# Optimization experiments

Measured on AMD Instinct MI355X. Metric: run time of the kernel, lower is better.

The kernel has to match this reference:

```python
import jax, jax.numpy as jnp
import numpy as np

B, IN, H, L = 128, 256, 1024, 256
nA, nB = H // 2, (H - 1) // 2        # pairs per A-layer / B-layer
LB = L // 2
LA = L - LB                           # A layers come first when L is odd
PI = float(np.pi)


def setup_inputs() -> dict:
    key = jax.random.key(0)
    ks = jax.random.split(key, 14)
    u = lambda k, shp: jax.random.uniform(k, shp, minval=-PI, maxval=PI)
    return {
        "inputsR": jax.random.normal(ks[0], (B, IN), dtype=jnp.float32),
        "inputsI": jax.random.normal(ks[1], (B, IN), dtype=jnp.float32),
        "stateR": jax.random.normal(ks[2], (B, H), dtype=jnp.float32),
        "stateI": jax.random.normal(ks[3], (B, H), dtype=jnp.float32),
        # CLinear params (init_scale=0.01 inside RNNCellCmplx)
        "weightR": 0.01 * jax.random.normal(ks[4], (H, IN), dtype=jnp.float32),
        "weightI": 0.01 * jax.random.normal(ks[5], (H, IN), dtype=jnp.float32),
        "biasR": 0.01 * jax.random.normal(ks[6], (H,), dtype=jnp.float32),
        "biasI": 0.01 * jax.random.normal(ks[7], (H,), dtype=jnp.float32),
        # Clements mesh angles, uniform(-pi, pi)
        "angleA0": u(ks[8], (LA, nA)),
        "angleA1": u(ks[9], (LA, nA)),
        "angleB0": u(ks[10], (LB, nB)),
        "angleB1": u(ks[11], (LB, nB)),
        # diagonal phase + modReLU bias (both init to zero)
        "omega": jnp.zeros((H,), dtype=jnp.float32),
        "mod_bias": jnp.zeros((H,), dtype=jnp.float32),
    }


def _mzi(ar, ai, br, bi, th0, th1):
    """PSDC MZI on channel pairs: phase shifter e^{i*th0} on arm a, then a
    directional coupler with coupling angle th1 (unitary 2x2)."""
    c0, s0 = jnp.cos(th0), jnp.sin(th0)
    pr = c0 * ar - s0 * ai          # p = e^{i th0} * a
    pi_ = s0 * ar + c0 * ai
    c, s = jnp.cos(th1), jnp.sin(th1)
    oar = c * pr - s * bi           # a' = cos*p + i sin*b
    oai = c * pi_ + s * br
    obr = c * br - s * pi_          # b' = i sin*p + cos*b
    obi = c * bi + s * pr
    return oar, oai, obr, obi


def _layerA(xr, xi, t0, t1):
    Bs, N = xr.shape
    oar, oai, obr, obi = _mzi(xr[:, 0::2], xi[:, 0::2], xr[:, 1::2], xi[:, 1::2], t0, t1)
    xr = jnp.stack([oar, obr], axis=-1).reshape(Bs, N)
    xi = jnp.stack([oai, obi], axis=-1).reshape(Bs, N)
    return xr, xi


def _layerB(xr, xi, t0, t1):
    Bs, N = xr.shape  # pairs (1,2),(3,4),... ; channels 0 and N-1 pass through
    oar, oai, obr, obi = _mzi(xr[:, 1:-1:2], xi[:, 1:-1:2], xr[:, 2::2], xi[:, 2::2], t0, t1)
    midr = jnp.stack([oar, obr], axis=-1).reshape(Bs, N - 2)
    midi = jnp.stack([oai, obi], axis=-1).reshape(Bs, N - 2)
    xr = jnp.concatenate([xr[:, :1], midr, xr[:, -1:]], axis=1)
    xi = jnp.concatenate([xi[:, :1], midi, xi[:, -1:]], axis=1)
    return xr, xi


def _clements(xr, xi, A0, A1, B0, B1):
    def step(carry, ang):
        cr, ci = carry
        a0, a1, b0, b1 = ang
        cr, ci = _layerA(cr, ci, a0, a1)
        cr, ci = _layerB(cr, ci, b0, b1)
        return (cr, ci), None
    (xr, xi), _ = jax.lax.scan(step, (xr, xi), (A0[:LB], A1[:LB], B0, B1))
    for k in range(LB, LA):  # trailing A layer when num_layers is odd (static)
        xr, xi = _layerA(xr, xi, A0[k], A1[k])
    return xr, xi


def _forward(inputsR, inputsI, stateR, stateI, weightR, weightI, biasR, biasI,
             angleA0, angleA1, angleB0, angleB1, omega, mod_bias):
    # CLinear: complex y = W x + b
    ihR = inputsR @ weightR.T - inputsI @ weightI.T + biasR
    ihI = inputsR @ weightI.T + inputsI @ weightR.T + biasI
    # Clements unitary mesh on hidden state
    hr, hi = _clements(stateR, stateI, angleA0, angleA1, angleB0, angleB1)
    # diagonal phase e^{i omega}
    co, so = jnp.cos(omega), jnp.sin(omega)
    hhR = co * hr - so * hi
    hhI = so * hr + co * hi
    # complex add
    zr = ihR + hhR
    zi = ihI + hhI
    # modReLU: relu(|z| + b) * z / |z|
    mag = jnp.sqrt(zr * zr + zi * zi)
    scale = jax.nn.relu(mag + mod_bias) / jnp.maximum(mag, 1e-8)
    return jnp.stack([scale * zr, scale * zi])  # (2, B, H)


def reference(inputsR, inputsI, stateR, stateI, weightR, weightI, biasR, biasI,
              angleA0, angleA1, angleB0, angleB1, omega, mod_bias):
    return _forward(inputsR, inputsI, stateR, stateI, weightR, weightI, biasR, biasI,
                    angleA0, angleA1, angleB0, angleB1, omega, mod_bias)
```

## Files before the change

kernel.cpp:

```cpp
#include <hip/hip_runtime.h>
#include <math.h>

typedef float v2 __attribute__((ext_vector_type(2)));

#define NBATCH 128
#define NIN    256
#define NH     1024
#define NSTEPS 128
#define NB     511

#define TAB_F4_PER_L 1024
#define IH_OFF (NSTEPS * TAB_F4_PER_L * 4)

#define GEMM_BLOCKS 256
#define TRIG_BLOCKS 512

static __device__ __forceinline__ v2 to2(float a, float b) { v2 r; r.x = a; r.y = b; return r; }

__global__ __launch_bounds__(256) void prep_kernel(
    const float* __restrict__ inR, const float* __restrict__ inI,
    const float* __restrict__ wR,  const float* __restrict__ wI,
    const float* __restrict__ biasR, const float* __restrict__ biasI,
    const float* __restrict__ A0, const float* __restrict__ A1,
    const float* __restrict__ B0, const float* __restrict__ B1,
    float* __restrict__ ws)
{
    __shared__ v2 xs[256][17];
    __shared__ v2 wsh[32][34];

    if (blockIdx.x >= GEMM_BLOCKS) {
        int idx = (blockIdx.x - GEMM_BLOCKS) * 256 + threadIdx.x;
        int l = idx >> 10;
        int s = idx & 1023;
        int j = s >> 8, g = s & 255;
        float a0, a1;
        bool ident = false;
        if (j < 2) {
            int p = 2 * g + j;
            a0 = A0[l * 512 + p]; a1 = A1[l * 512 + p];
        } else {
            int p = 2 * g + (j - 2);
            if (p < NB) { a0 = B0[l * NB + p]; a1 = B1[l * NB + p]; }
            else ident = true;
        }
        float4 v;
        if (ident) v = make_float4(1.f, 0.f, 1.f, 0.f);
        else {
            float s0, c0, s1, c1;
            __sincosf(a0, &s0, &c0);
            __sincosf(a1, &s1, &c1);
            v = make_float4(c0, s0, c1, s1);
        }
        ((float4*)ws)[l * TAB_F4_PER_L + j * 256 + g] = v;
        return;
    }

    const int ht = blockIdx.x >> 3, bt = blockIdx.x & 7;
    const int h0 = ht * 32, b0 = bt * 16;
    const int tid = threadIdx.x;

    {
        int b = tid >> 4, k4 = tid & 15;
#pragma unroll
        for (int p = 0; p < 4; ++p) {
            int k0 = p * 64 + k4 * 4;
            float4 vr = *(const float4*)(inR + (b0 + b) * NIN + k0);
            float4 vi = *(const float4*)(inI + (b0 + b) * NIN + k0);
            xs[k0 + 0][b] = to2(vr.x, vi.x);
            xs[k0 + 1][b] = to2(vr.y, vi.y);
            xs[k0 + 2][b] = to2(vr.z, vi.z);
            xs[k0 + 3][b] = to2(vr.w, vi.w);
        }
    }

    const int hg = tid & 15, bl = tid >> 4;
    v2 acc0 = to2(0.f, 0.f), acc1 = to2(0.f, 0.f);

    for (int c = 0; c < 8; ++c) {
        __syncthreads();
        {
            int hh = tid >> 3, k4 = tid & 7;
            float4 vr = *(const float4*)(wR + (h0 + hh) * NIN + c * 32 + k4 * 4);
            float4 vi = *(const float4*)(wI + (h0 + hh) * NIN + c * 32 + k4 * 4);
            wsh[k4 * 4 + 0][hh] = to2(vr.x, vi.x);
            wsh[k4 * 4 + 1][hh] = to2(vr.y, vi.y);
            wsh[k4 * 4 + 2][hh] = to2(vr.z, vi.z);
            wsh[k4 * 4 + 3][hh] = to2(vr.w, vi.w);
        }
        __syncthreads();
#pragma unroll
        for (int k = 0; k < 32; ++k) {
            float4 wv = *(const float4*)&wsh[k][hg * 2];
            v2 w0 = to2(wv.x, wv.y), w1 = to2(wv.z, wv.w);
            v2 xv = xs[c * 32 + k][bl];
            acc0 += to2(xv.x, xv.x) * w0 + to2(xv.y, xv.y) * to2(-w0.y, w0.x);
            acc1 += to2(xv.x, xv.x) * w1 + to2(xv.y, xv.y) * to2(-w1.y, w1.x);
        }
    }
    int h = h0 + hg * 2, b = b0 + bl;
    acc0 += to2(biasR[h], biasI[h]);
    acc1 += to2(biasR[h + 1], biasI[h + 1]);
    ((float4*)(ws + IH_OFF))[b * 512 + (h >> 1)] =
        make_float4(acc0.x, acc0.y, acc1.x, acc1.y);
}

__device__ __forceinline__ void mzi(const float4 t, v2& a, v2& b)
{
    v2 P  = to2(t.x, t.y) * to2(a.x, a.x) + to2(-t.y, t.x) * to2(a.y, a.y);
    v2 na = to2(t.z, t.z) * P + to2(-t.w, t.w) * to2(b.y, b.x);
    b     = to2(t.z, t.z) * b + to2(-t.w, t.w) * to2(P.y, P.x);
    a = na;
}

__device__ __forceinline__ void stage_layer(const float4* __restrict__ tab, int l,
                                            float4* dst, int w, int lane)
{
    const float4* src = tab + l * TAB_F4_PER_L + w * 256 + lane;
    float4* d = dst + w * 256;
#pragma unroll
    for (int c = 0; c < 4; ++c) {
        __builtin_amdgcn_global_load_lds(
            (const __attribute__((address_space(1))) unsigned int*)(src + c * 64),
            (__attribute__((address_space(3))) unsigned int*)(d + c * 64),
            16, 0, 0);
    }
}

__global__ __launch_bounds__(256, 1) void mesh_kernel(
    const float* __restrict__ stateR, const float* __restrict__ stateI,
    const float* __restrict__ omega,  const float* __restrict__ mod_bias,
    const float* __restrict__ ws, float* __restrict__ out)
{
    const int b = blockIdx.x;
    const int g = threadIdx.x;
    const int lane = g & 63;
    const int w = g >> 6;
    const float4* tab = (const float4*)ws;

    __shared__ float4 tb[3][TAB_F4_PER_L];
    __shared__ v2 sx0[2][3];
    __shared__ v2 sx3[2][3];

    v2 x[4];
    {
        float4 r = *(const float4*)(stateR + b * NH + 4 * g);
        float4 i = *(const float4*)(stateI + b * NH + 4 * g);
        x[0] = to2(r.x, i.x);
        x[1] = to2(r.y, i.y);
        x[2] = to2(r.z, i.z);
        x[3] = to2(r.w, i.w);
    }

    stage_layer(tab, 0, &tb[0][0], w, lane);
    stage_layer(tab, 1, &tb[1][0], w, lane);
    __asm__ volatile("s_waitcnt vmcnt(0)" ::: "memory");
    __syncthreads();

    float4 T0 = tb[0][g], T1 = tb[0][256 + g], T2 = tb[0][512 + g], T3 = tb[0][768 + g];
    float4 TL = tb[0][768 + ((g - 1) & 255)];
    if (g == 0) TL = make_float4(1.f, 0.f, 1.f, 0.f);

    int s = 0;
    for (int l = 0; l < NSTEPS; ++l) {
        const int par = l & 1;
        mzi(T0, x[0], x[1]);
        mzi(T1, x[2], x[3]);
        if (lane == 0 && w > 0)  sx0[par][w - 1] = x[0];
        if (lane == 63 && w < 3) sx3[par][w] = x[3];
        __asm__ volatile("s_waitcnt vmcnt(0) lgkmcnt(0)" ::: "memory");
        __builtin_amdgcn_s_barrier();
        __asm__ volatile("" ::: "memory");

        int s2 = s + 2; if (s2 >= 3) s2 -= 3;
        if (l + 2 < NSTEPS) stage_layer(tab, l + 2, &tb[s2][0], w, lane);

        float rcr = __shfl_down(x[0].x, 1, 64);
        float rci = __shfl_down(x[0].y, 1, 64);
        float lcr = __shfl_up(x[3].x, 1, 64);
        float lci = __shfl_up(x[3].y, 1, 64);
        if (lane == 63 && w < 3) { v2 t = sx0[par][w]; rcr = t.x; rci = t.y; }
        if (lane == 0 && w > 0)  { v2 t = sx3[par][w - 1]; lcr = t.x; lci = t.y; }

        mzi(T2, x[1], x[2]);

        int s1 = s + 1; if (s1 >= 3) s1 -= 3;
        float4 N0, N1, N2, N3, NL;
        if (l + 1 < NSTEPS) {
            N0 = tb[s1][g];
            N1 = tb[s1][256 + g];
            N2 = tb[s1][512 + g];
            N3 = tb[s1][768 + g];
            NL = tb[s1][768 + ((g - 1) & 255)];
        } else {
            N0 = N1 = N2 = N3 = NL = make_float4(1.f, 0.f, 1.f, 0.f);
        }

        {
            v2 P = to2(T3.x, T3.y) * to2(x[3].x, x[3].x) + to2(-T3.y, T3.x) * to2(x[3].y, x[3].y);
            x[3] = to2(T3.z, T3.z) * P + to2(-T3.w, T3.w) * to2(rci, rcr);
        }
        {
            v2 P = to2(TL.x, TL.y) * to2(lcr, lcr) + to2(-TL.y, TL.x) * to2(lci, lci);
            x[0] = to2(TL.z, TL.z) * x[0] + to2(-TL.w, TL.w) * to2(P.y, P.x);
        }

        T0 = N0; T1 = N1; T2 = N2; T3 = N3; TL = NL;
        if (g == 0) TL = make_float4(1.f, 0.f, 1.f, 0.f);
        s = s1;
    }

    float4 o4 = *(const float4*)(omega + 4 * g);
    float4 m4 = *(const float4*)(mod_bias + 4 * g);
    const float4* ihp = (const float4*)(ws + IH_OFF) + b * 512 + 2 * g;
    float4 ih0 = ihp[0], ih1 = ihp[1];

    float om[4] = { o4.x, o4.y, o4.z, o4.w };
    float mb[4] = { m4.x, m4.y, m4.z, m4.w };
    float ihr[4] = { ih0.x, ih0.z, ih1.x, ih1.z };
    float ihi[4] = { ih0.y, ih0.w, ih1.y, ih1.w };
    float oR[4], oI[4];
#pragma unroll
    for (int j = 0; j < 4; ++j) {
        float so, co;
        __sincosf(om[j], &so, &co);
        float zr = ihr[j] + co * x[j].x - so * x[j].y;
        float zi = ihi[j] + so * x[j].x + co * x[j].y;
        float mag = sqrtf(zr * zr + zi * zi);
        float sc = fmaxf(mag + mb[j], 0.f) / fmaxf(mag, 1e-8f);
        oR[j] = sc * zr;
        oI[j] = sc * zi;
    }
    *(float4*)(out + b * NH + 4 * g) = make_float4(oR[0], oR[1], oR[2], oR[3]);
    *(float4*)(out + NBATCH * NH + b * NH + 4 * g) = make_float4(oI[0], oI[1], oI[2], oI[3]);
}

extern "C" void kernel_launch(void* const* d_in, const int* in_sizes, int n_in,
                              void* d_out, int out_size, void* d_ws, size_t ws_size,
                              hipStream_t stream)
{
    const float* inputsR = (const float*)d_in[0];
    const float* inputsI = (const float*)d_in[1];
    const float* stateR  = (const float*)d_in[2];
    const float* stateI  = (const float*)d_in[3];
    const float* weightR = (const float*)d_in[4];
    const float* weightI = (const float*)d_in[5];
    const float* biasR   = (const float*)d_in[6];
    const float* biasI   = (const float*)d_in[7];
    const float* angleA0 = (const float*)d_in[8];
    const float* angleA1 = (const float*)d_in[9];
    const float* angleB0 = (const float*)d_in[10];
    const float* angleB1 = (const float*)d_in[11];
    const float* omega   = (const float*)d_in[12];
    const float* mod_b   = (const float*)d_in[13];
    float* ws = (float*)d_ws;
    float* out = (float*)d_out;

    hipLaunchKernelGGL(prep_kernel, dim3(GEMM_BLOCKS + TRIG_BLOCKS), dim3(256),
                       0, stream, inputsR, inputsI, weightR, weightI,
                       biasR, biasI, angleA0, angleA1, angleB0, angleB1, ws);
    hipLaunchKernelGGL(mesh_kernel, dim3(NBATCH), dim3(256), 0, stream,
                       stateR, stateI, omega, mod_b, ws, out);
}
```

Baseline: 181.1 us.

## Deepen angle-table prefetch to three layers with partial vmcnt waits

The mesh kernel now keeps three layers of angle tables in flight through global_load_lds and waits with vmcnt(4) instead of vmcnt(0), so each step no longer has to drain every outstanding load. The barrier moves after the third MZI so that compute overlaps the wait, and the stage for layer l+3 is issued into the buffer just consumed. The aim is to hide global-load latency on the serial 128-step loop. It relies on the partial waitcnt count matching exactly four loads per stage; near the end it issues redundant loads of the last layer to keep that count constant.

```diff
diff --git a/kernel.cpp b/kernel.cpp
--- a/kernel.cpp
+++ b/kernel.cpp
@@ -112,19 +112,29 @@
     a = na;
 }
 
-__device__ __forceinline__ void stage_layer(const float4* __restrict__ tab, int l,
-                                            float4* dst, int w, int lane)
-{
-    const float4* src = tab + l * TAB_F4_PER_L + w * 256 + lane;
-    float4* d = dst + w * 256;
-#pragma unroll
-    for (int c = 0; c < 4; ++c) {
-        __builtin_amdgcn_global_load_lds(
-            (const __attribute__((address_space(1))) unsigned int*)(src + c * 64),
-            (__attribute__((address_space(3))) unsigned int*)(d + c * 64),
-            16, 0, 0);
-    }
-}
+#define STAGE(l, s)                                                          \
+    do {                                                                     \
+        _Pragma("unroll") for (int _c = 0; _c < 4; ++_c) {                   \
+            const float4* _src = tab + (size_t)(l) * TAB_F4_PER_L            \
+                                 + (w * 4 + _c) * 64 + lane;                 \
+            float4* _dst = &tbuf[s][(w * 4 + _c) * 64];                      \
+            __builtin_amdgcn_global_load_lds(                                \
+                (const __attribute__((address_space(1))) unsigned int*)_src, \
+                (__attribute__((address_space(3))) unsigned int*)_dst,       \
+                16, 0, 0);                                                   \
+        }                                                                    \
+    } while (0)
+
+#define READT(T0_, T1_, T2_, T3_, TL_, l)                                    \
+    do {                                                                     \
+        int _s = (l) % 3;                                                    \
+        T0_ = tbuf[_s][g];                                                   \
+        T1_ = tbuf[_s][256 + g];                                             \
+        T2_ = tbuf[_s][512 + g];                                             \
+        T3_ = tbuf[_s][768 + g];                                             \
+        TL_ = tbuf[_s][768 + ((g - 1) & 255)];                               \
+        if (g == 0) TL_ = make_float4(1.f, 0.f, 1.f, 0.f);                   \
+    } while (0)
 
 __global__ __launch_bounds__(256, 1) void mesh_kernel(
     const float* __restrict__ stateR, const float* __restrict__ stateI,
@@ -137,7 +147,7 @@
     const int w = g >> 6;
     const float4* tab = (const float4*)ws;
 
-    __shared__ float4 tb[3][TAB_F4_PER_L];
+    __shared__ float4 tbuf[3][TAB_F4_PER_L];
     __shared__ v2 sx0[2][3];
     __shared__ v2 sx3[2][3];
 
@@ -151,50 +161,40 @@
         x[3] = to2(r.w, i.w);
     }
 
-    stage_layer(tab, 0, &tb[0][0], w, lane);
-    stage_layer(tab, 1, &tb[1][0], w, lane);
-    __asm__ volatile("s_waitcnt vmcnt(0)" ::: "memory");
-    __syncthreads();
-
-    float4 T0 = tb[0][g], T1 = tb[0][256 + g], T2 = tb[0][512 + g], T3 = tb[0][768 + g];
-    float4 TL = tb[0][768 + ((g - 1) & 255)];
-    if (g == 0) TL = make_float4(1.f, 0.f, 1.f, 0.f);
-
-    int s = 0;
+    STAGE(0, 0);
+    STAGE(1, 1);
+    STAGE(2, 2);
+    asm volatile("s_waitcnt vmcnt(8)" ::: "memory");
+    __builtin_amdgcn_s_barrier();
+    __builtin_amdgcn_sched_barrier(0);
+
+    float4 T0, T1, T2, T3, TL;
+    READT(T0, T1, T2, T3, TL, 0);
+
     for (int l = 0; l < NSTEPS; ++l) {
         const int par = l & 1;
         mzi(T0, x[0], x[1]);
         mzi(T1, x[2], x[3]);
         if (lane == 0 && w > 0)  sx0[par][w - 1] = x[0];
         if (lane == 63 && w < 3) sx3[par][w] = x[3];
-        __asm__ volatile("s_waitcnt vmcnt(0) lgkmcnt(0)" ::: "memory");
-        __builtin_amdgcn_s_barrier();
-        __asm__ volatile("" ::: "memory");
-
-        int s2 = s + 2; if (s2 >= 3) s2 -= 3;
-        if (l + 2 < NSTEPS) stage_layer(tab, l + 2, &tb[s2][0], w, lane);
-
         float rcr = __shfl_down(x[0].x, 1, 64);
         float rci = __shfl_down(x[0].y, 1, 64);
         float lcr = __shfl_up(x[3].x, 1, 64);
         float lci = __shfl_up(x[3].y, 1, 64);
+        mzi(T2, x[1], x[2]);
+        asm volatile("s_waitcnt vmcnt(4) lgkmcnt(0)" ::: "memory");
+        __builtin_amdgcn_s_barrier();
+        __builtin_amdgcn_sched_barrier(0);
+
+        float4 N0 = T0, N1 = T1, N2 = T2, N3 = T3, NL = TL;
+        if (l + 1 < NSTEPS) READT(N0, N1, N2, N3, NL, l + 1);
+        {
+            int ls = (l + 3 < NSTEPS) ? l + 3 : NSTEPS - 1;
+            STAGE(ls, l % 3);
+        }
         if (lane == 63 && w < 3) { v2 t = sx0[par][w]; rcr = t.x; rci = t.y; }
         if (lane == 0 && w > 0)  { v2 t = sx3[par][w - 1]; lcr = t.x; lci = t.y; }
 
-        mzi(T2, x[1], x[2]);
-
-        int s1 = s + 1; if (s1 >= 3) s1 -= 3;
-        float4 N0, N1, N2, N3, NL;
-        if (l + 1 < NSTEPS) {
-            N0 = tb[s1][g];
-            N1 = tb[s1][256 + g];
-            N2 = tb[s1][512 + g];
-            N3 = tb[s1][768 + g];
-            NL = tb[s1][768 + ((g - 1) & 255)];
-        } else {
-            N0 = N1 = N2 = N3 = NL = make_float4(1.f, 0.f, 1.f, 0.f);
-        }
-
         {
             v2 P = to2(T3.x, T3.y) * to2(x[3].x, x[3].x) + to2(-T3.y, T3.x) * to2(x[3].y, x[3].y);
             x[3] = to2(T3.z, T3.z) * P + to2(-T3.w, T3.w) * to2(rci, rcr);
@@ -205,9 +205,9 @@
         }
 
         T0 = N0; T1 = N1; T2 = N2; T3 = N3; TL = NL;
-        if (g == 0) TL = make_float4(1.f, 0.f, 1.f, 0.f);
-        s = s1;
-    }
+    }
+
+    asm volatile("s_waitcnt vmcnt(0)" ::: "memory");
 
     float4 o4 = *(const float4*)(omega + 4 * g);
     float4 m4 = *(const float4*)(mod_bias + 4 * g);
```

Result: faster. 167.7 us (-7.4%).
